# Kernel optimization log

Hardware: AMD Instinct MI355X
Metric: run time of the kernel (lower is better)

## Reference

```python
import jax, jax.numpy as jnp
import numpy as np

N = 50000          # num_assets / nodes
E = 1_600_000      # edges (avg degree 32)
F = 128            # num_features
R = 4              # num_relations
H = 1              # heads
O1, O2 = 15, 10    # RGATConv out_channels (hard-coded in module)
NEG_SLOPE = 0.2    # leaky_relu slope in RGATConv
BN_EPS = 1e-5


def setup_inputs() -> dict:
    key = jax.random.key(0)
    ks = jax.random.split(key, 24)
    s = 0.1
    return {
        "node_emb": jax.random.normal(ks[0], (N, F), jnp.float32),
        "edge_index": jax.random.randint(ks[1], (2, E), 0, N),
        "edge_types": jax.random.randint(ks[2], (E,), 0, R),
        "edge_attr": jax.random.normal(ks[3], (E, 1), jnp.float32),
        # RGATConv layer 1 params
        "W1": jax.random.normal(ks[4], (R, F, H * O1), jnp.float32) * s,
        "q1": jax.random.normal(ks[5], (H * O1, H), jnp.float32) * s,
        "k1": jax.random.normal(ks[6], (H * O1, H), jnp.float32) * s,
        "e1": jax.random.normal(ks[7], (H * O1, H), jnp.float32) * s,
        "We1": jax.random.normal(ks[8], (1, H * O1), jnp.float32) * s,  # lin_edge
        "b1": jax.random.normal(ks[9], (H * O1,), jnp.float32) * s,
        # RGATConv layer 2 params
        "W2": jax.random.normal(ks[10], (R, H * O1, H * O2), jnp.float32) * s,
        "q2": jax.random.normal(ks[11], (H * O2, H), jnp.float32) * s,
        "k2": jax.random.normal(ks[12], (H * O2, H), jnp.float32) * s,
        "e2": jax.random.normal(ks[13], (H * O2, H), jnp.float32) * s,
        "We2": jax.random.normal(ks[14], (1, H * O2), jnp.float32) * s,
        "b2": jax.random.normal(ks[15], (O2,), jnp.float32) * s,
        # BatchNorm affine params
        "g1": 1.0 + jax.random.normal(ks[16], (H * O1,), jnp.float32) * 0.05,
        "beta1": jax.random.normal(ks[17], (H * O1,), jnp.float32) * 0.05,
        "g2": 1.0 + jax.random.normal(ks[18], (O2,), jnp.float32) * 0.05,
        "beta2": jax.random.normal(ks[19], (O2,), jnp.float32) * 0.05,
        # head Linear(10, 1)
        "w_head": jax.random.normal(ks[20], (O2, 1), jnp.float32) * s,
        "b_head": jax.random.normal(ks[21], (1,), jnp.float32) * s,
    }


def _segment_softmax(alpha, dst, n):
    amax = jax.ops.segment_max(alpha, dst, num_segments=n)
    ex = jnp.exp(alpha - amax[dst])
    denom = jax.ops.segment_sum(ex, dst, num_segments=n)
    return ex / (denom[dst] + 1e-16)


def _rgat(x, src, dst, etype, eattr, W, q, k, e, We, b, heads, out_ch, concat):
    n = x.shape[0]
    # per-relation transform of all nodes, then gather per-edge (same math as
    # PyG's per-edge bmm with W[edge_type])
    xt = jnp.einsum('nf,rfo->nro', x, W)            # [N, R, H*O]
    out_i = xt[dst, etype]                          # [E, H*O] (target)
    out_j = xt[src, etype]                          # [E, H*O] (source)
    alpha = out_i @ q + out_j @ k + (eattr @ We) @ e  # [E, H]
    alpha = jax.nn.leaky_relu(alpha, NEG_SLOPE)
    alpha = _segment_softmax(alpha, dst, n)          # across-relation softmax over dst
    msg = (alpha[:, :, None] * out_j.reshape(-1, heads, out_ch)).reshape(-1, heads * out_ch)
    agg = jax.ops.segment_sum(msg, dst, num_segments=n)
    if not concat:
        agg = agg.reshape(n, heads, out_ch).mean(axis=1)
    return agg + b


def _bn_elu(x, g, beta):
    # training-mode BatchNorm1d (batch statistics, biased variance) + ELU
    mu = x.mean(axis=0)
    var = x.var(axis=0)
    xh = (x - mu) / jnp.sqrt(var + BN_EPS)
    return jax.nn.elu(xh * g + beta)


def reference(node_emb, edge_index, edge_types, edge_attr,
              W1, q1, k1, e1, We1, b1,
              W2, q2, k2, e2, We2, b2,
              g1, beta1, g2, beta2, w_head, b_head):
    src, dst = edge_index[0], edge_index[1]
    x = _rgat(node_emb, src, dst, edge_types, edge_attr,
              W1, q1, k1, e1, We1, b1, H, O1, True)
    x = _bn_elu(x, g1, beta1)
    x = _rgat(x, src, dst, edge_types, edge_attr,
              W2, q2, k2, e2, We2, b2, H, O2, False)
    x = _bn_elu(x, g2, beta2)
    return x @ w_head + b_head                       # [N, 1]
```

## Files before the change

### kernel.cpp

```cpp
#include <hip/hip_runtime.h>


typedef unsigned short ushort_t;
typedef unsigned int uint_t;
typedef __attribute__((ext_vector_type(8))) short bf16x8;
typedef __attribute__((ext_vector_type(4))) float f32x4;

#define NEG_SLOPE 0.2f
#define BN_EPS 1e-5f
#define NBUCK 512
#define REC 4096

__device__ __forceinline__ float bf2f(ushort_t u) {
    return __uint_as_float(((uint_t)u) << 16);
}
__device__ __forceinline__ ushort_t f2bf(float f) {
    uint_t x = __float_as_uint(f);
    x += 0x7FFFu + ((x >> 16) & 1u);
    return (ushort_t)(x >> 16);
}
__device__ __forceinline__ float h2f(ushort_t u) {
    _Float16 h = __builtin_bit_cast(_Float16, u);
    return (float)h;
}
__device__ __forceinline__ ushort_t f2h(float f) {
    _Float16 h = (_Float16)f;
    return __builtin_bit_cast(ushort_t, h);
}
__device__ __forceinline__ float loadf(const void* p, int i, int isb) {
    return isb ? bf2f(((const ushort_t*)p)[i]) : ((const float*)p)[i];
}
__device__ __forceinline__ float sel4(float a0, float a1, float a2, float a3, int et) {
    float lo = (et == 1) ? a1 : a0;
    float hi = (et == 3) ? a3 : a2;
    return (et >= 2) ? hi : lo;
}

__global__ __launch_bounds__(256) void k_prep(const uint_t* __restrict__ x,
                                              const void* __restrict__ W1,
                                              const void* __restrict__ W2,
                                              const void* __restrict__ q1b,
                                              const void* __restrict__ k1b,
                                              const void* __restrict__ We1,
                                              const void* __restrict__ e1v,
                                              const void* __restrict__ We2,
                                              const void* __restrict__ e2v,
                                              int* __restrict__ dflag,
                                              int* __restrict__ bcur,
                                              float* __restrict__ stats1,
                                              float* __restrict__ stats2,
                                              float* __restrict__ cbuf,
                                              ushort_t* __restrict__ Wsw,
                                              float* __restrict__ Wf2, int cap) {
    __shared__ int cnt;
    int t = threadIdx.x;
    if (t == 0) cnt = 0;
    __syncthreads();
    uint_t u = x[t * 37];
    uint_t lo_exp = (u >> 7) & 0xFF;
    atomicAdd(&cnt, (lo_exp >= 96 && lo_exp <= 150) ? 1 : 0);
    __syncthreads();
    int isb = (cnt > 192) ? 1 : 0;
    if (blockIdx.x == 0) {
        if (t == 0) {
            dflag[0] = isb;
            float c1 = 0.f;
            for (int o = 0; o < 15; ++o) c1 += loadf(We1, o, isb) * loadf(e1v, o, isb);
            float c2 = 0.f;
            for (int o = 0; o < 10; ++o) c2 += loadf(We2, o, isb) * loadf(e2v, o, isb);
            cbuf[0] = c1;
            cbuf[1] = c2;
        }
        for (int i = t; i < NBUCK; i += 256) bcur[i] = i * cap;
        stats1[t] = 0.f;
        stats2[t] = 0.f;
        for (int idx = t; idx < 15 * 40; idx += 256) {
            int f = idx / 40, j = idx % 40, r = j / 10, o = j % 10;
            Wf2[idx] = loadf(W2, (r * 15 + f) * 10 + o, isb);
        }
    }
    for (int idx = blockIdx.x * 256 + t; idx < 20 * 64 * 8; idx += gridDim.x * 256) {
        int j = idx & 7, lane = (idx >> 3) & 63, fr = idx >> 9;
        int ks = fr / 5, ct = fr % 5;
        int k = ks * 32 + (lane >> 4) * 8 + j;
        int c = ct * 16 + (lane & 15);
        float v = 0.f;
        if (c < 64) {
            int r = c >> 4, o = c & 15;
            if (o < 15) {
                v = loadf(W1, (r * 128 + k) * 15 + o, isb);
            } else {
                float s = 0.f;
#pragma unroll
                for (int oo = 0; oo < 15; ++oo)
                    s += loadf(W1, (r * 128 + k) * 15 + oo, isb) * loadf(k1b, oo, isb);
                v = s;
            }
        } else if (c < 68) {
            int r = c - 64;
            float s = 0.f;
#pragma unroll
            for (int oo = 0; oo < 15; ++oo)
                s += loadf(W1, (r * 128 + k) * 15 + oo, isb) * loadf(q1b, oo, isb);
            v = s;
        }
        Wsw[idx] = f2bf(v);
    }
}

__global__ __launch_bounds__(512) void k_bucket(const int* __restrict__ ei,
                                                const int* __restrict__ et,
                                                const void* __restrict__ ea,
                                                const int* __restrict__ flag,
                                                int* __restrict__ bcur,
                                                int2* __restrict__ tmp,
                                                int E, int npb) {
    extern __shared__ int2 srec[];
    __shared__ int cnt[NBUCK];
    __shared__ int lofs[NBUCK + 1];
    __shared__ int gpos[NBUCK];
    int t = threadIdx.x;
    int isb = flag[0];
    cnt[t] = 0;
    __syncthreads();
    int e0 = blockIdx.x * REC;
    for (int i = 0; i < REC / 512; ++i) {
        int e = e0 + i * 512 + t;
        if (e < E) atomicAdd(&cnt[ei[E + e] / npb], 1);
    }
    __syncthreads();
    int myc = cnt[t];
    for (int off = 1; off < NBUCK; off <<= 1) {
        int v = (t >= off) ? cnt[t - off] : 0;
        __syncthreads();
        cnt[t] += v;
        __syncthreads();
    }
    lofs[t] = cnt[t] - myc;
    if (t == NBUCK - 1) lofs[NBUCK] = cnt[NBUCK - 1];
    __syncthreads();
    cnt[t] = lofs[t];
    __syncthreads();
    for (int i = 0; i < REC / 512; ++i) {
        int e = e0 + i * 512 + t;
        if (e < E) {
            int d = ei[E + e];
            int b = d / npb;
            int ldst = d - b * npb;
            int idx = atomicAdd(&cnt[b], 1);
            int2 r;
            r.x = (int)((uint_t)ei[e] | ((uint_t)et[e] << 23) | ((uint_t)ldst << 25));
            r.y = (int)(((uint_t)b << 16) | (uint_t)f2bf(loadf(ea, e, isb)));
            srec[idx] = r;
        }
    }
    __syncthreads();
    int c_b = lofs[t + 1] - lofs[t];
    gpos[t] = atomicAdd(&bcur[t], c_b);
    __syncthreads();
    int total = lofs[NBUCK];
    for (int i = t; i < total; i += 512) {
        int2 rr = srec[i];
        int bkt = (int)(((uint_t)rr.y) >> 16);
        tmp[gpos[bkt] + (i - lofs[bkt])] = rr;
    }
}

__global__ __launch_bounds__(256) void k_b2csr(const int2* __restrict__ tmp,
                                               const int* __restrict__ bcur,
                                               int* __restrict__ rs,
                                               int* __restrict__ re,
                                               int2* __restrict__ ebuf,
                                               int N, int npb, int cap) {
    __shared__ int cnt[128];
    __shared__ int lofs[129];
    int b = blockIdx.x, t = threadIdx.x;
    int s0 = b * cap;
    int s1 = bcur[b];
    if (t < 128) cnt[t] = 0;
    __syncthreads();
    for (int p = s0 + t; p < s1; p += 256) {
        uint_t x = (uint_t)tmp[p].x;
        atomicAdd(&cnt[(x >> 25) & 0x7F], 1);
    }
    __syncthreads();
    int myc = (t < 128) ? cnt[t] : 0;
    for (int off = 1; off < 128; off <<= 1) {
        int v = (t >= off && t < 128) ? cnt[t - off] : 0;
        __syncthreads();
        if (t < 128) cnt[t] += v;
        __syncthreads();
    }
    if (t < 128) {
        lofs[t] = cnt[t] - myc;
        if (t == 127) lofs[128] = cnt[127];
    }
    __syncthreads();
    int node0 = b * npb;
    if (t < npb && node0 + t < N) {
        rs[node0 + t] = s0 + lofs[t];
        re[node0 + t] = s0 + lofs[t + 1];
    }
    if (t < 128) cnt[t] = lofs[t];
    __syncthreads();
    for (int p = s0 + t; p < s1; p += 256) {
        int2 r = tmp[p];
        uint_t x = (uint_t)r.x;
        int ldst = (x >> 25) & 0x7F;
        int idx = atomicAdd(&cnt[ldst], 1);
        int2 o;
        o.x = (int)(x & 0x7FFFFF) | (((int)(x >> 23) & 3) << 20);
        o.y = (int)(((uint_t)(node0 + ldst) << 16) |
                    ((uint_t)r.y & 0xFFFFu));
        ebuf[s0 + idx] = o;
    }
}

__global__ __launch_bounds__(256) void k_t1(const void* __restrict__ xin,
                                            const ushort_t* __restrict__ Wsw,
                                            const int* __restrict__ flag,
                                            ushort_t* __restrict__ xt,
                                            float* __restrict__ dq,
                                            int N, int ntiles, int nwaves) {
    int isb = flag[0];
    int lane = threadIdx.x & 63;
    int gw = blockIdx.x * 4 + (threadIdx.x >> 6);
    bf16x8 bfr[20];
    const uint4* wq = (const uint4*)Wsw;
#pragma unroll
    for (int fr = 0; fr < 20; ++fr)
        bfr[fr] = __builtin_bit_cast(bf16x8, wq[fr * 64 + lane]);
    int row = lane & 15, quad = lane >> 4;
    for (int tile = gw; tile < ntiles; tile += nwaves) {
        int n0 = tile * 16;
        f32x4 acc[5];
#pragma unroll
        for (int ct = 0; ct < 5; ++ct) acc[ct] = (f32x4){0.f, 0.f, 0.f, 0.f};
        int nA = n0 + row;
        if (nA >= N) nA = N - 1;
#pragma unroll
        for (int ks = 0; ks < 4; ++ks) {
            bf16x8 af;
            if (isb) {
                uint4 u = *(const uint4*)((const ushort_t*)xin + (size_t)nA * 128 + ks * 32 + quad * 8);
                af = __builtin_bit_cast(bf16x8, u);
            } else {
                const float* xf = (const float*)xin + (size_t)nA * 128 + ks * 32 + quad * 8;
#pragma unroll
                for (int j = 0; j < 8; ++j) af[j] = (short)f2bf(xf[j]);
            }
#pragma unroll
            for (int ct = 0; ct < 5; ++ct)
                acc[ct] = __builtin_amdgcn_mfma_f32_16x16x32_bf16(af, bfr[ks * 5 + ct], acc[ct], 0, 0, 0);
        }
#pragma unroll
        for (int i = 0; i < 4; ++i) {
            int n = n0 + quad * 4 + i;
            if (n < N) {
#pragma unroll
                for (int ct = 0; ct < 4; ++ct) {
                    float val = acc[ct][i];
                    ushort_t bits = (row == 15) ? f2h(val) : f2bf(val);
                    xt[(size_t)n * 64 + ct * 16 + row] = bits;
                }
                if (row < 4) dq[n * 4 + row] = acc[4][i];
            }
        }
    }
}

__global__ __launch_bounds__(256) void k_t2(const float* __restrict__ in,
                                            const float* __restrict__ stats,
                                            const void* __restrict__ g,
                                            const void* __restrict__ beta,
                                            const float* __restrict__ Wf,
                                            const void* __restrict__ qb,
                                            const void* __restrict__ kb,
                                            const int* __restrict__ flag,
                                            ushort_t* __restrict__ xt,
                                            float* __restrict__ dq, int N) {
    int isb = flag[0];
    int t = threadIdx.x;
    int lane = t & 63;
    int r = t >> 6;
    int n = blockIdx.x * 64 + lane;
    if (n >= N) return;
    float invN = 1.f / (float)N;
    float v[15];
#pragma unroll
    for (int c = 0; c < 15; ++c) {
        float mean = stats[c * 16] * invN;
        float var = stats[c * 16 + 8] * invN - mean * mean;
        float inv = rsqrtf(var + BN_EPS);
        float h = (in[(size_t)n * 15 + c] - mean) * inv * loadf(g, c, isb) + loadf(beta, c, isb);
        v[c] = h > 0.f ? h : expm1f(h);
    }
    float acc[10];
#pragma unroll
    for (int o = 0; o < 10; ++o) acc[o] = 0.f;
#pragma unroll
    for (int f = 0; f < 15; ++f) {
        const float* wp = Wf + f * 40 + r * 10;
#pragma unroll
        for (int o = 0; o < 10; ++o) acc[o] += v[f] * wp[o];
    }
    float sq = 0.f, sk = 0.f;
#pragma unroll
    for (int o = 0; o < 10; ++o) {
        sq += acc[o] * loadf(qb, o, isb);
        sk += acc[o] * loadf(kb, o, isb);
    }
    dq[n * 4 + r] = sq;
    ushort_t* xr = xt + (size_t)n * 64 + r * 16;
    uint_t pk[8];
#pragma unroll
    for (int j = 0; j < 5; ++j)
        pk[j] = (uint_t)f2bf(acc[2 * j]) | ((uint_t)f2bf(acc[2 * j + 1]) << 16);
    pk[5] = 0; pk[6] = 0;
    pk[7] = ((uint_t)f2h(sk)) << 16;
    *(uint4*)(xr)     = make_uint4(pk[0], pk[1], pk[2], pk[3]);
    *(uint4*)(xr + 8) = make_uint4(pk[4], pk[5], pk[6], pk[7]);
}

template <int O>
__global__ __launch_bounds__(256) void k_gather(const int* __restrict__ rs,
                                                const int* __restrict__ re,
                                                const int2* __restrict__ ebuf,
                                                const ushort_t* __restrict__ xt,
                                                const float* __restrict__ dq,
                                                const float* __restrict__ cp,
                                                const void* __restrict__ bb,
                                                const int* __restrict__ flag,
                                                float* __restrict__ out, int N) {
    int isb = flag[0];
    int lane = threadIdx.x & 63;
    int w = threadIdx.x >> 6;
    int n = blockIdx.x * 4 + w;
    if (n >= N) return;
    int start = rs[n], end = re[n];
    int ch = lane & 15;
    int gb = lane & 48;
    bool hi15 = (ch == 15);
    float c = cp[0];
    float q0 = dq[n * 4], q1 = dq[n * 4 + 1], q2 = dq[n * 4 + 2], q3 = dq[n * 4 + 3];
    float acc = 0.f, s = 0.f;
    int p = start + (gb >> 4);
    for (; p + 12 < end; p += 16) {
        int2 v0 = ebuf[p];
        int2 v1 = ebuf[p + 4];
        int2 v2 = ebuf[p + 8];
        int2 v3 = ebuf[p + 12];
        ushort_t u0 = xt[(size_t)((v0.x & 0xFFFFF) * 4 + (v0.x >> 20)) * 16 + ch];
        ushort_t u1 = xt[(size_t)((v1.x & 0xFFFFF) * 4 + (v1.x >> 20)) * 16 + ch];
        ushort_t u2 = xt[(size_t)((v2.x & 0xFFFFF) * 4 + (v2.x >> 20)) * 16 + ch];
        ushort_t u3 = xt[(size_t)((v3.x & 0xFFFFF) * 4 + (v3.x >> 20)) * 16 + ch];
        float x0 = hi15 ? h2f(u0) : bf2f(u0);
        float x1 = hi15 ? h2f(u1) : bf2f(u1);
        float x2 = hi15 ? h2f(u2) : bf2f(u2);
        float x3 = hi15 ? h2f(u3) : bf2f(u3);
        float dk0 = __shfl(x0, gb + 15, 64);
        float dk1 = __shfl(x1, gb + 15, 64);
        float dk2 = __shfl(x2, gb + 15, 64);
        float dk3 = __shfl(x3, gb + 15, 64);
        float a0 = sel4(q0, q1, q2, q3, v0.x >> 20) + dk0 + c * bf2f((ushort_t)(v0.y & 0xFFFFu));
        float a1 = sel4(q0, q1, q2, q3, v1.x >> 20) + dk1 + c * bf2f((ushort_t)(v1.y & 0xFFFFu));
        float a2 = sel4(q0, q1, q2, q3, v2.x >> 20) + dk2 + c * bf2f((ushort_t)(v2.y & 0xFFFFu));
        float a3 = sel4(q0, q1, q2, q3, v3.x >> 20) + dk3 + c * bf2f((ushort_t)(v3.y & 0xFFFFu));
        float e0 = __expf(fmaxf(a0, NEG_SLOPE * a0));
        float e1 = __expf(fmaxf(a1, NEG_SLOPE * a1));
        float e2 = __expf(fmaxf(a2, NEG_SLOPE * a2));
        float e3 = __expf(fmaxf(a3, NEG_SLOPE * a3));
        s += (e0 + e1) + (e2 + e3);
        acc += e0 * x0;
        acc += e1 * x1;
        acc += e2 * x2;
        acc += e3 * x3;
    }
    for (; p < end; p += 4) {
        int2 v = ebuf[p];
        ushort_t u = xt[(size_t)((v.x & 0xFFFFF) * 4 + (v.x >> 20)) * 16 + ch];
        float x = hi15 ? h2f(u) : bf2f(u);
        float dk = __shfl(x, gb + 15, 64);
        float a = sel4(q0, q1, q2, q3, v.x >> 20) + dk + c * bf2f((ushort_t)(v.y & 0xFFFFu));
        float e = __expf(fmaxf(a, NEG_SLOPE * a));
        acc += e * x;
        s += e;
    }
    s   += __shfl_xor(s, 16, 64);
    s   += __shfl_xor(s, 32, 64);
    acc += __shfl_xor(acc, 16, 64);
    acc += __shfl_xor(acc, 32, 64);
    if (lane < O) out[(size_t)n * O + lane] = acc / (s + 1e-16f) + loadf(bb, lane, isb);
}

template <int C>
__global__ __launch_bounds__(256) void k_bnstats(const float* __restrict__ in,
                                                 float* __restrict__ S, int N) {
    int t = threadIdx.x;
    int ch = t & 15, rg = t >> 4;
    float s1 = 0.f, s2 = 0.f;
    int row0 = blockIdx.x * 256;
    int rowEnd = row0 + 256;
    if (rowEnd > N) rowEnd = N;
    if (ch < C) {
        for (int r = row0 + rg; r < rowEnd; r += 16) {
            float v = in[(size_t)r * C + ch];
            s1 += v;
            s2 += v * v;
        }
    }
    __shared__ float L1[256], L2[256];
    L1[t] = s1; L2[t] = s2;
    __syncthreads();
    for (int k = 128; k >= 16; k >>= 1) {
        if (t < k) { L1[t] += L1[t + k]; L2[t] += L2[t + k]; }
        __syncthreads();
    }
    if (t < C) {
        atomicAdd(&S[t * 16], L1[t]);
        atomicAdd(&S[t * 16 + 8], L2[t]);
    }
}

__global__ __launch_bounds__(256) void k_head(const float* __restrict__ in,
                                              const float* __restrict__ stats,
                                              const void* __restrict__ g,
                                              const void* __restrict__ beta,
                                              const void* __restrict__ wh,
                                              const void* __restrict__ bh,
                                              const int* __restrict__ flag,
                                              void* __restrict__ out, int N) {
    int isb = flag[0];
    int n = blockIdx.x * 256 + threadIdx.x;
    if (n >= N) return;
    float invN = 1.f / (float)N;
    float r = loadf(bh, 0, isb);
#pragma unroll
    for (int c = 0; c < 10; ++c) {
        float mean = stats[c * 16] * invN;
        float var = stats[c * 16 + 8] * invN - mean * mean;
        float inv = rsqrtf(var + BN_EPS);
        float h = (in[(size_t)n * 10 + c] - mean) * inv * loadf(g, c, isb) + loadf(beta, c, isb);
        float e = h > 0.f ? h : expm1f(h);
        r += e * loadf(wh, c, isb);
    }
    if (isb) ((ushort_t*)out)[n] = f2bf(r);
    else     ((float*)out)[n] = r;
}

extern "C" void kernel_launch(void* const* d_in, const int* in_sizes, int n_in,
                              void* d_out, int out_size, void* d_ws, size_t ws_size,
                              hipStream_t stream) {
    const void* node_emb  = d_in[0];
    const int*  edge_index = (const int*)d_in[1];
    const int*  edge_types = (const int*)d_in[2];
    const void* edge_attr = d_in[3];
    const void* W1  = d_in[4];
    const void* q1  = d_in[5];
    const void* k1  = d_in[6];
    const void* e1  = d_in[7];
    const void* We1 = d_in[8];
    const void* b1  = d_in[9];
    const void* W2  = d_in[10];
    const void* q2  = d_in[11];
    const void* k2  = d_in[12];
    const void* e2  = d_in[13];
    const void* We2 = d_in[14];
    const void* b2  = d_in[15];
    const void* g1  = d_in[16];
    const void* beta1 = d_in[17];
    const void* g2  = d_in[18];
    const void* beta2 = d_in[19];
    const void* w_head = d_in[20];
    const void* b_head = d_in[21];

    int N = in_sizes[0] / 128;
    int E = in_sizes[1] / 2;
    int npb = (N + NBUCK - 1) / NBUCK;
    int nbuck = (N + npb - 1) / npb;
    int cap = E / nbuck + 512;
    size_t slots = (size_t)nbuck * cap;

    char* ws = (char*)d_ws;
    size_t off = 0;
    auto alloc = [&](size_t bytes) -> void* {
        void* p = ws + off;
        off = (off + bytes + 255) & ~(size_t)255;
        return p;
    };
    int*   rs      = (int*)alloc((size_t)N * 4);
    int*   re      = (int*)alloc((size_t)N * 4);
    int*   bcur    = (int*)alloc((NBUCK) * 4);
    int*   dflag   = (int*)alloc(256);
    float* cbuf    = (float*)alloc(256);
    int2*  ebuf    = (int2*)alloc(slots * 8);
    size_t big = (size_t)N * 64 * 2;
    if (slots * 8 > big) big = slots * 8;
    ushort_t* xt1  = (ushort_t*)alloc(big);
    int2*  etmp    = (int2*)xt1;
    float* dq1     = (float*)alloc((size_t)N * 16);
    float* out1    = (float*)alloc((size_t)N * 15 * 4);
    float* stats1  = (float*)alloc(256 * 4);
    float* stats2  = (float*)alloc(256 * 4);
    ushort_t* Wsw  = (ushort_t*)alloc(20 * 64 * 8 * 2);
    float* Wf2     = (float*)alloc(600 * 4);
    ushort_t* xt2 = xt1;
    float* dq2  = dq1;
    float* out2 = out1;

    int NB_N = (N + 255) / 256;
    int NB_T2 = (N + 63) / 64;
    int NB_G = (N + 3) / 4;
    int NB_B = (E + REC - 1) / REC;
    int ntiles = (N + 15) / 16;
    int NB_T1 = 391;
    int nwaves = NB_T1 * 4;

    k_prep<<<40, 256, 0, stream>>>((const uint_t*)node_emb, W1, W2, q1, k1,
                                   We1, e1, We2, e2,
                                   dflag, bcur, stats1, stats2, cbuf, Wsw, Wf2, cap);
    k_bucket<<<NB_B, 512, REC * sizeof(int2), stream>>>(edge_index, edge_types, edge_attr,
                                                        dflag, bcur, etmp, E, npb);
    k_b2csr<<<nbuck, 256, 0, stream>>>(etmp, bcur, rs, re, ebuf, N, npb, cap);

    k_t1<<<NB_T1, 256, 0, stream>>>(node_emb, Wsw, dflag, xt1, dq1, N, ntiles, nwaves);
    k_gather<15><<<NB_G, 256, 0, stream>>>(rs, re, ebuf, xt1, dq1, cbuf, b1, dflag, out1, N);
    k_bnstats<15><<<NB_N, 256, 0, stream>>>(out1, stats1, N);
    k_t2<<<NB_T2, 256, 0, stream>>>(out1, stats1, g1, beta1, Wf2, q2, k2, dflag, xt2, dq2, N);
    k_gather<10><<<NB_G, 256, 0, stream>>>(rs, re, ebuf, xt2, dq2, cbuf + 1, b2, dflag, out2, N);
    k_bnstats<10><<<NB_N, 256, 0, stream>>>(out2, stats2, N);
    k_head<<<NB_N, 256, 0, stream>>>(out2, stats2, g2, beta2, w_head, b_head, dflag, d_out, N);
}
```

Before: 300.5 us.

## Compute edge attention once per lane and broadcast weights to channel groups

Reorganizes the edge gather kernel so each of the 64 lanes scores one edge at a time: it loads that edge's key term, computes the exp once, and the row index and weight are then broadcast by shuffle to the 16-lane channel groups for the feature accumulation. Before, every lane in a 16-channel group recomputed the same exp and leaky-relu, and the key came in through a per-edge shuffle. The aim is to remove that 16x redundant transcendental and ALU work. In exchange it adds an extra scattered load per edge for the key column, more shuffles, and a masked tail path. Since the average degree is below 64, most nodes will run the tail path.

After: 304.8 us. Within noise of the previous version (+1.4%).

```diff
diff --git a/kernel.cpp b/kernel.cpp
--- a/kernel.cpp
+++ b/kernel.cpp
@@ -339,55 +339,54 @@
     if (n >= N) return;
     int start = rs[n], end = re[n];
     int ch = lane & 15;
-    int gb = lane & 48;
-    bool hi15 = (ch == 15);
+    int g = lane >> 4;
     float c = cp[0];
     float q0 = dq[n * 4], q1 = dq[n * 4 + 1], q2 = dq[n * 4 + 2], q3 = dq[n * 4 + 3];
     float acc = 0.f, s = 0.f;
-    int p = start + (gb >> 4);
-    for (; p + 12 < end; p += 16) {
-        int2 v0 = ebuf[p];
-        int2 v1 = ebuf[p + 4];
-        int2 v2 = ebuf[p + 8];
-        int2 v3 = ebuf[p + 12];
-        ushort_t u0 = xt[(size_t)((v0.x & 0xFFFFF) * 4 + (v0.x >> 20)) * 16 + ch];
-        ushort_t u1 = xt[(size_t)((v1.x & 0xFFFFF) * 4 + (v1.x >> 20)) * 16 + ch];
-        ushort_t u2 = xt[(size_t)((v2.x & 0xFFFFF) * 4 + (v2.x >> 20)) * 16 + ch];
-        ushort_t u3 = xt[(size_t)((v3.x & 0xFFFFF) * 4 + (v3.x >> 20)) * 16 + ch];
-        float x0 = hi15 ? h2f(u0) : bf2f(u0);
-        float x1 = hi15 ? h2f(u1) : bf2f(u1);
-        float x2 = hi15 ? h2f(u2) : bf2f(u2);
-        float x3 = hi15 ? h2f(u3) : bf2f(u3);
-        float dk0 = __shfl(x0, gb + 15, 64);
-        float dk1 = __shfl(x1, gb + 15, 64);
-        float dk2 = __shfl(x2, gb + 15, 64);
-        float dk3 = __shfl(x3, gb + 15, 64);
-        float a0 = sel4(q0, q1, q2, q3, v0.x >> 20) + dk0 + c * bf2f((ushort_t)(v0.y & 0xFFFFu));
-        float a1 = sel4(q0, q1, q2, q3, v1.x >> 20) + dk1 + c * bf2f((ushort_t)(v1.y & 0xFFFFu));
-        float a2 = sel4(q0, q1, q2, q3, v2.x >> 20) + dk2 + c * bf2f((ushort_t)(v2.y & 0xFFFFu));
-        float a3 = sel4(q0, q1, q2, q3, v3.x >> 20) + dk3 + c * bf2f((ushort_t)(v3.y & 0xFFFFu));
-        float e0 = __expf(fmaxf(a0, NEG_SLOPE * a0));
-        float e1 = __expf(fmaxf(a1, NEG_SLOPE * a1));
-        float e2 = __expf(fmaxf(a2, NEG_SLOPE * a2));
-        float e3 = __expf(fmaxf(a3, NEG_SLOPE * a3));
-        s += (e0 + e1) + (e2 + e3);
-        acc += e0 * x0;
-        acc += e1 * x1;
-        acc += e2 * x2;
-        acc += e3 * x3;
-    }
-    for (; p < end; p += 4) {
-        int2 v = ebuf[p];
-        ushort_t u = xt[(size_t)((v.x & 0xFFFFF) * 4 + (v.x >> 20)) * 16 + ch];
-        float x = hi15 ? h2f(u) : bf2f(u);
-        float dk = __shfl(x, gb + 15, 64);
-        float a = sel4(q0, q1, q2, q3, v.x >> 20) + dk + c * bf2f((ushort_t)(v.y & 0xFFFFu));
+    int base = start;
+    for (; base + 64 <= end; base += 64) {
+        int2 rec = ebuf[base + lane];
+        int row = (rec.x & 0xFFFFF) * 4 + (rec.x >> 20);
+        float dkv = h2f(xt[(size_t)row * 16 + 15]);
+        float a = sel4(q0, q1, q2, q3, rec.x >> 20) + dkv +
+                  c * bf2f((ushort_t)(rec.y & 0xFFFFu));
         float e = __expf(fmaxf(a, NEG_SLOPE * a));
-        acc += e * x;
         s += e;
-    }
-    s   += __shfl_xor(s, 16, 64);
-    s   += __shfl_xor(s, 32, 64);
+#pragma unroll
+        for (int j = 0; j < 16; ++j) {
+            int sl = 4 * j + g;
+            int rowj = __shfl(row, sl, 64);
+            float ej = __shfl(e, sl, 64);
+            acc += ej * bf2f(xt[(size_t)rowj * 16 + ch]);
+        }
+    }
+    if (base < end) {
+        int clen = end - base;
+        int idx = base + lane;
+        int idc = (idx < end) ? idx : (end - 1);
+        int2 rec = ebuf[idc];
+        int row = (rec.x & 0xFFFFF) * 4 + (rec.x >> 20);
+        float dkv = h2f(xt[(size_t)row * 16 + 15]);
+        float a = sel4(q0, q1, q2, q3, rec.x >> 20) + dkv +
+                  c * bf2f((ushort_t)(rec.y & 0xFFFFu));
+        float e = (idx < end) ? __expf(fmaxf(a, NEG_SLOPE * a)) : 0.f;
+        s += e;
+#pragma unroll
+        for (int j = 0; j < 16; ++j) {
+            if (4 * j < clen) {
+                int sl = 4 * j + g;
+                int rowj = __shfl(row, sl, 64);
+                float ej = __shfl(e, sl, 64);
+                acc += ej * bf2f(xt[(size_t)rowj * 16 + ch]);
+            }
+        }
+    }
+    s += __shfl_xor(s, 1, 64);
+    s += __shfl_xor(s, 2, 64);
+    s += __shfl_xor(s, 4, 64);
+    s += __shfl_xor(s, 8, 64);
+    s += __shfl_xor(s, 16, 64);
+    s += __shfl_xor(s, 32, 64);
     acc += __shfl_xor(acc, 16, 64);
     acc += __shfl_xor(acc, 32, 64);
     if (lane < O) out[(size_t)n * O + lane] = acc / (s + 1e-16f) + loadf(bb, lane, isb);
```
